# Kernel optimization log

Measured on AMD Instinct MI355X. Metric: run time of the kernel, lower is better.

## Reference

```python
import jax, jax.numpy as jnp
import numpy as np
import math

B, H, L, N, CD = 16, 512, 2048, 64, 128
BN_EPS = 1e-5


def setup_inputs() -> dict:
    key = jax.random.key(0)
    ks = jax.random.split(key, 12)
    x = jax.random.normal(ks[0], (B, H, L), jnp.float32)
    cond = jax.random.normal(ks[1], (B, CD), jnp.float32)
    # input Linear(H, H)
    linear_w = jax.random.normal(ks[2], (H, H), jnp.float32) * (1.0 / math.sqrt(H))
    linear_b = jax.random.normal(ks[3], (H,), jnp.float32) * 0.01
    # DSSM params (torch init: log_dt ~ U[log dt_min, log dt_max])
    log_dt = jax.random.uniform(ks[4], (H,), jnp.float32) * (math.log(0.1) - math.log(0.001)) + math.log(0.001)
    C_ri = jax.random.normal(ks[5], (H, N, 2), jnp.float32)  # view_as_real of complex C
    log_A_real = jnp.full((H, N), jnp.log(0.5), jnp.float32)
    A_imag = jnp.broadcast_to(math.pi * jnp.arange(N, dtype=jnp.float32), (H, N))
    D = jax.random.normal(ks[6], (H,), jnp.float32)
    # FiLM adaptor Linear(CD, 2H)
    film_w = jax.random.normal(ks[7], (2 * H, CD), jnp.float32) * (1.0 / math.sqrt(CD))
    film_b = jax.random.normal(ks[8], (2 * H,), jnp.float32) * 0.01
    # depthwise 1x1 residual conv (groups=H, bias=False) -> per-channel scale
    res_w = jax.random.normal(ks[9], (H,), jnp.float32)
    return {"x": x, "cond": cond, "linear_w": linear_w, "linear_b": linear_b,
            "log_dt": log_dt, "C_ri": C_ri, "log_A_real": log_A_real,
            "A_imag": A_imag, "D": D, "film_w": film_w, "film_b": film_b,
            "res_w": res_w}


def _s4_kernel(log_dt, C_ri, log_A_real, A_imag, length):
    dt = jnp.exp(log_dt)                       # [H]
    C = C_ri[..., 0] + 1j * C_ri[..., 1]       # [H, N] complex
    A = -jnp.exp(log_A_real) + 1j * A_imag     # [H, N] complex
    dtA = A * dt[:, None]                      # [H, N]
    t = jnp.arange(length, dtype=jnp.float32)
    P = dtA[:, :, None] * t                    # [H, N, L] complex
    Cm = C * (jnp.exp(dtA) - 1.0) / A          # [H, N]
    K = 2.0 * jnp.einsum('hn,hnl->hl', Cm, jnp.exp(P)).real  # [H, L]
    return K


def reference(x, cond, linear_w, linear_b, log_dt, C_ri, log_A_real, A_imag, D,
              film_w, film_b, res_w):
    # --- linear over channel dim (B H L -> B L H -> linear -> B H L) ---
    h = jnp.einsum('bhl,gh->bgl', x, linear_w) + linear_b[None, :, None]
    h = jax.nn.gelu(h, approximate=False)  # torch.nn.GELU default (erf)
    # --- DSSM: full-length group (forward passes length=None) ---
    K = _s4_kernel(log_dt, C_ri, log_A_real, A_imag, L)     # [H, L]
    n_fft = 2 * L
    k_f = jnp.fft.rfft(K, n=n_fft)                           # [H, Lf]
    u_f = jnp.fft.rfft(h, n=n_fft)                           # [B, H, Lf]
    y = jnp.fft.irfft(u_f * k_f[None], n=n_fft)[..., :L]     # [B, H, L]
    y = y + h * D[None, :, None]                             # D skip
    # --- FiLM: BatchNorm1d(affine=False, batch stats) then scale/shift ---
    gb = cond @ film_w.T + film_b                            # [B, 2H]
    g, b = gb[:, :H], gb[:, H:]
    mean = jnp.mean(y, axis=(0, 2), keepdims=True)
    var = jnp.var(y, axis=(0, 2), keepdims=True)             # biased, as torch BN
    y = (y - mean) * jax.lax.rsqrt(var + BN_EPS)
    y = y * g[:, :, None] + b[:, :, None]
    y = jax.nn.gelu(y, approximate=False)
    # --- depthwise 1x1 residual ---
    return y + x * res_w[None, :, None]
```

## Files before the change

### kernel.cpp

```cpp
#include <hip/hip_runtime.h>
#include <math.h>

#define B_ 16
#define H_ 512
#define L_ 2048
#define N_ 64
#define CD_ 128
#define KSTRIDE 2112

typedef unsigned int u32;
typedef unsigned short u16;
typedef __attribute__((ext_vector_type(8))) short bf16x8;
typedef __attribute__((ext_vector_type(4))) float f32x4;

__device__ __forceinline__ float gelu_f(float v) {
    return 0.5f * v * (1.0f + erff(v * 0.70710678118654752f));
}
__device__ __forceinline__ float bf2f(u16 b) {
    union { u32 u; float f; } c; c.u = ((u32)b) << 16; return c.f;
}
__device__ __forceinline__ u16 f2bf(float f) {
    union { float f; u32 u; } c; c.f = f;
    u32 u = c.u;
    return (u16)((u + 0x7FFFu + ((u >> 16) & 1u)) >> 16);
}
__device__ __forceinline__ u32 pack2(float a, float b) {
    u32 r;
    asm("v_cvt_pk_bf16_f32 %0, %1, %2" : "=v"(r) : "v"(a), "v"(b));
    return r;
}
__device__ __forceinline__ float2 cmul(float2 a, float2 b) {
    return make_float2(a.x * b.x - a.y * b.y, a.x * b.y + a.y * b.x);
}

__global__ void k_fill(float* __restrict__ out, int n, float val) {
    int i = blockIdx.x * 256 + threadIdx.x;
    if (i < n) out[i] = val;
}

__global__ __launch_bounds__(128) void k_prepW(const float* __restrict__ W,
                                               u16* __restrict__ Wb) {
    int g = blockIdx.x, t = threadIdx.x;
    float4 v = ((const float4*)(W + (size_t)g * H_))[t];
    u32* dst = (u32*)(Wb + (size_t)g * H_);
    dst[t * 2]     = pack2(v.x, v.y);
    dst[t * 2 + 1] = pack2(v.z, v.w);
}

__global__ __launch_bounds__(256) void k_K4(
    const float* __restrict__ log_dt, const float* __restrict__ C_ri,
    const float* __restrict__ log_A_real, const float* __restrict__ A_imag,
    u16* __restrict__ Krv) {
    int h = blockIdx.x, t = threadIdx.x;
    __shared__ float2 P1[N_][8], P8[N_][4], P32[N_][8], P256[N_][8], Cs[N_];
    if (t < N_) {
        int n = t;
        float dt = expf(log_dt[h]);
        float a_re = -expf(log_A_real[h * N_ + n]);
        float a_im = A_imag[h * N_ + n];
        float dre = a_re * dt, dim = a_im * dt;
        float er = expf(dre);
        float s, c;
        sincosf(dim, &s, &c);
        float2 E1 = make_float2(er * c, er * s);
        float num_re = E1.x - 1.0f, num_im = E1.y;
        float den = a_re * a_re + a_im * a_im;
        float q_re = (num_re * a_re + num_im * a_im) / den;
        float q_im = (num_im * a_re - num_re * a_im) / den;
        float Cr = C_ri[(h * N_ + n) * 2 + 0], Ci = C_ri[(h * N_ + n) * 2 + 1];
        Cs[n] = make_float2(Cr * q_re - Ci * q_im, Cr * q_im + Ci * q_re);
        float2 w = make_float2(1.f, 0.f);
        #pragma unroll
        for (int i = 0; i < 8; ++i) { P1[n][i] = w; w = cmul(w, E1); }
        float2 E8 = w; w = make_float2(1.f, 0.f);
        #pragma unroll
        for (int i = 0; i < 4; ++i) { P8[n][i] = w; w = cmul(w, E8); }
        float2 E32 = w; w = make_float2(1.f, 0.f);
        #pragma unroll
        for (int i = 0; i < 8; ++i) { P32[n][i] = w; w = cmul(w, E32); }
        float2 E256 = w; w = make_float2(1.f, 0.f);
        #pragma unroll
        for (int i = 0; i < 8; ++i) { P256[n][i] = w; w = cmul(w, E256); }
    }
    __syncthreads();
    int qh = t >> 5, ql = (t >> 2) & 7, rh = t & 3;
    float acc[8] = {};
    for (int n = 0; n < N_; ++n) {
        float2 a = cmul(Cs[n], P256[n][qh]);
        a = cmul(a, P32[n][ql]);
        a = cmul(a, P8[n][rh]);
        #pragma unroll
        for (int j = 0; j < 8; ++j) {
            float2 e = P1[n][j];
            acc[j] += a.x * e.x - a.y * e.y;
        }
    }
    u16* Krow = Krv + (size_t)h * KSTRIDE;
    uint4 w4;
    w4.x = pack2(2.0f * acc[7], 2.0f * acc[6]);
    w4.y = pack2(2.0f * acc[5], 2.0f * acc[4]);
    w4.z = pack2(2.0f * acc[3], 2.0f * acc[2]);
    w4.w = pack2(2.0f * acc[1], 2.0f * acc[0]);
    *(uint4*)&Krow[2040 - 8 * t] = w4;
    if (t < 8) {
        uint4 z = {0u, 0u, 0u, 0u};
        *(uint4*)&Krow[2048 + 8 * t] = z;
    }
}

__global__ __launch_bounds__(512, 4) void k_linear7(
    const float* __restrict__ x, const u16* __restrict__ Wb,
    const float* __restrict__ bias, u16* __restrict__ hb16) {
    int b  = blockIdx.z;
    int g0 = blockIdx.y * 128;
    int l0 = blockIdx.x * 128;
    __shared__ __align__(16) char sm[34816];
    u16* Wp = (u16*)sm;
    u16* Bl = (u16*)(sm + 16384);
    int t = threadIdx.x;
    int lane = t & 63, wv = t >> 6;
    int n = lane & 15, kg = lane >> 4;
    int wr = wv >> 2, wc = wv & 3;
    int lr  = t & 127, kq = t >> 7;
    int wrow = t >> 2, woct = t & 3;

    f32x4 acc[4][2];
    #pragma unroll
    for (int m = 0; m < 4; ++m)
        #pragma unroll
        for (int q = 0; q < 2; ++q) acc[m][q] = (f32x4){0.f, 0.f, 0.f, 0.f};

    const float* xcol = x + (size_t)b * H_ * L_ + l0 + lr;
    const u32* wsrc = (const u32*)(Wb + (size_t)(g0 + wrow) * H_);

    float cx[16], nx[16];
    uint4 cwq[2], nwq[2];
    #pragma unroll
    for (int e = 0; e < 16; ++e) cx[e] = xcol[(size_t)(kq * 16 + e) * L_];
    #pragma unroll
    for (int j = 0; j < 2; ++j)
        cwq[j] = *(const uint4*)&wsrc[(woct * 2 + j) * 4];

    #pragma unroll
    for (int S = 0; S < 8; ++S) {
        if (S) __syncthreads();
        {
            u32 px[8];
            #pragma unroll
            for (int e = 0; e < 8; ++e) px[e] = pack2(cx[2 * e], cx[2 * e + 1]);
            uint4 u0 = {px[0], px[1], px[2], px[3]};
            uint4 u1 = {px[4], px[5], px[6], px[7]};
            *(uint4*)((char*)Bl + lr * 144 + kq * 32)      = u0;
            *(uint4*)((char*)Bl + lr * 144 + kq * 32 + 16) = u1;
        }
        #pragma unroll
        for (int j = 0; j < 2; ++j) {
            int oct = woct * 2 + j;
            *(uint4*)((char*)Wp + wrow * 128 + ((oct * 16) ^ ((wrow & 7) << 4))) = cwq[j];
        }
        __syncthreads();
        if (S < 7) {
            int k0n = (S + 1) * 64;
            #pragma unroll
            for (int e = 0; e < 16; ++e) nx[e] = xcol[(size_t)(k0n + kq * 16 + e) * L_];
            #pragma unroll
            for (int j = 0; j < 2; ++j)
                nwq[j] = *(const uint4*)&wsrc[k0n / 2 + (woct * 2 + j) * 4];
        }
        #pragma unroll
        for (int ks = 0; ks < 2; ++ks) {
            bf16x8 af[4], bfr[2];
            #pragma unroll
            for (int m = 0; m < 4; ++m) {
                int row = wr * 64 + m * 16 + n;
                af[m] = *(const bf16x8*)((const char*)Wp + row * 128 +
                         ((ks * 64 + kg * 16) ^ ((row & 7) << 4)));
            }
            #pragma unroll
            for (int q = 0; q < 2; ++q)
                bfr[q] = *(const bf16x8*)((const char*)Bl +
                          (wc * 32 + q * 16 + n) * 144 + ks * 64 + kg * 16);
            #pragma unroll
            for (int m = 0; m < 4; ++m)
                #pragma unroll
                for (int q = 0; q < 2; ++q)
                    acc[m][q] = __builtin_amdgcn_mfma_f32_16x16x32_bf16(
                        af[m], bfr[q], acc[m][q], 0, 0, 0);
        }
        if (S < 7) {
            #pragma unroll
            for (int e = 0; e < 16; ++e) cx[e] = nx[e];
            cwq[0] = nwq[0]; cwq[1] = nwq[1];
        }
    }

    __syncthreads();
    u16* Yt = (u16*)sm;
    #pragma unroll
    for (int m = 0; m < 4; ++m) {
        #pragma unroll
        for (int r = 0; r < 4; ++r) {
            int grow = wr * 64 + m * 16 + kg * 4 + r;
            float bi = bias[g0 + grow];
            float v0 = gelu_f(acc[m][0][r] + bi);
            float v1 = gelu_f(acc[m][1][r] + bi);
            u32 pr = pack2(v0, v1);
            Yt[grow * 128 + wc * 32 + n]      = (u16)(pr & 0xFFFFu);
            Yt[grow * 128 + wc * 32 + 16 + n] = (u16)(pr >> 16);
        }
    }
    __syncthreads();
    int rrow = t >> 4, c16 = t & 15;
    #pragma unroll
    for (int pass = 0; pass < 4; ++pass) {
        int row = rrow + 32 * pass;
        uint4 v = *(const uint4*)&Yt[row * 128 + c16 * 8];
        *(uint4*)&hb16[((size_t)b * H_ + g0 + row) * L_ + l0 + c16 * 8] = v;
    }
}

template<int E, bool DIAG, bool TAIL, bool LOAD>
__device__ __forceinline__ void cstep(const uint2* __restrict__ KD2, int& base,
    bf16x8 (&ring)[8], f32x4 (&accR)[8], const char* smem,
    int rowbase, u32 swz, int kg16, int& ja) {
    uint2 w01, w23;
    if (DIAG) {
        int b0 = base < 2047 ? base : 2047;
        int b1 = (base + 4) < 2047 ? (base + 4) : 2047;
        w01 = KD2[b0];
        w23 = KD2[b1];
        if (base > 2047)     { w01.x = 0u; w01.y = 0u; }
        if (base + 4 > 2047) { w23.x = 0u; w23.y = 0u; }
    } else {
        w01 = KD2[base];
        w23 = KD2[base + 4];
    }
    union { u32 u[4]; bf16x8 v; } bu;
    bu.u[0] = w01.x; bu.u[1] = w01.y; bu.u[2] = w23.x; bu.u[3] = w23.y;
    #pragma unroll
    for (int m = 0; m < 8; ++m)
        if (!TAIL || m >= E)
            accR[m] = __builtin_amdgcn_mfma_f32_16x16x32_bf16(
                ring[(m - E) & 7], bu.v, accR[m], 0, 0, 0);
    if (LOAD) {
        ring[(7 - E) & 7] = *(const bf16x8*)(smem + rowbase +
                            (((u32)(ja * 64 + kg16)) ^ swz));
        ja -= 1;
    }
    base -= 32;
}

template<bool DIAG, bool TAIL, bool LOAD>
__device__ __forceinline__ void cblock8(const uint2* __restrict__ KD2, int& base,
    bf16x8 (&ring)[8], f32x4 (&accR)[8], const char* smem,
    int rowbase, u32 swz, int kg16, int& ja) {
    cstep<0, DIAG,  TAIL, LOAD>(KD2, base, ring, accR, smem, rowbase, swz, kg16, ja);
    cstep<1, false, TAIL, LOAD>(KD2, base, ring, accR, smem, rowbase, swz, kg16, ja);
    cstep<2, false, TAIL, LOAD>(KD2, base, ring, accR, smem, rowbase, swz, kg16, ja);
    cstep<3, false, TAIL, LOAD>(KD2, base, ring, accR, smem, rowbase, swz, kg16, ja);
    cstep<4, false, TAIL, LOAD>(KD2, base, ring, accR, smem, rowbase, swz, kg16, ja);
    cstep<5, false, TAIL, LOAD>(KD2, base, ring, accR, smem, rowbase, swz, kg16, ja);
    cstep<6, false, TAIL, LOAD>(KD2, base, ring, accR, smem, rowbase, swz, kg16, ja);
    cstep<7, false, TAIL, LOAD>(KD2, base, ring, accR, smem, rowbase, swz, kg16, ja);
}

__global__ __launch_bounds__(512, 4) void k_conv_mfma(
    float* __restrict__ out, const u16* __restrict__ hb16,
    const u16* __restrict__ Krv, const float* __restrict__ Dp,
    const float* __restrict__ x, const float* __restrict__ cond,
    const float* __restrict__ film_w, const float* __restrict__ film_b,
    const float* __restrict__ res_w) {
    int g = blockIdx.x;
    __shared__ __align__(16) char smem[81920];
    uint2* KD2 = (uint2*)(smem + 65536);
    int t = threadIdx.x;
    int wv = t >> 6, lane = t & 63;
    int n = lane & 15, kg = lane >> 4;

    {
        const u16* Krow = Krv + (size_t)g * KSTRIDE;
        uint2 d0 = *(const uint2*)&Krow[4 * t];
        uint2 d1 = *(const uint2*)&Krow[4 * t + 4];
        u32 m12 = (d0.x >> 16) | (d0.y << 16);
        u32 m34 = (d0.y >> 16) | (d1.x << 16);
        u32 m56 = (d1.x >> 16) | (d1.y << 16);
        uint4 e01 = {d0.x, d0.y, m12, m34};
        uint4 e23 = {d0.y, d1.x, m34, m56};
        *(uint4*)&KD2[4 * t]     = e01;
        *(uint4*)&KD2[4 * t + 2] = e23;
    }
    #pragma unroll
    for (int b = 0; b < B_; ++b) {
        uint2 p2 = *(const uint2*)&hb16[((size_t)b * H_ + g) * L_ + t * 4];
        *(uint2*)(smem + b * 4096 + (((u32)(t * 8)) ^ ((b & 7) << 4))) = p2;
    }
    __syncthreads();

    const int p = wv & 1, q4 = wv >> 1;
    const int rowbase = n * 4096;
    const u32 swz = (u32)((n & 7) << 4);
    const int kg16 = kg * 16;
    const int bofs = 8 * kg - n;
    const int rrs[2] = {q4, 7 - q4};

    f32x4 acc[2][8];
    #pragma unroll
    for (int ri = 0; ri < 2; ++ri)
        #pragma unroll
        for (int m = 0; m < 8; ++m) acc[ri][m] = (f32x4){0.f, 0.f, 0.f, 0.f};

    #pragma unroll
    for (int ri = 0; ri < 2; ++ri) {
        const int rr = rrs[ri];
        const int k8 = rr * 8;
        bf16x8 ring[8];
        #pragma unroll
        for (int m = 0; m < 8; ++m)
            ring[m] = *(const bf16x8*)(smem + rowbase +
                      (((u32)((k8 + m) * 64 + kg16)) ^ swz));
        int base = 2047 - 16 * p + bofs;
        int ja = k8 - 1;
        if (rr == 0) {
            cblock8<true, true, false>(KD2, base, ring, acc[ri], smem, rowbase, swz, kg16, ja);
        } else {
            cblock8<true, false, true>(KD2, base, ring, acc[ri], smem, rowbase, swz, kg16, ja);
            for (int bi = 1; bi < rr; ++bi)
                cblock8<false, false, true>(KD2, base, ring, acc[ri], smem, rowbase, swz, kg16, ja);
            cblock8<false, true, false>(KD2, base, ring, acc[ri], smem, rowbase, swz, kg16, ja);
        }
    }

    __syncthreads();
    float Dg = Dp[g];
    float sum = 0.f, sq = 0.f;
    #pragma unroll
    for (int ri = 0; ri < 2; ++ri) {
        #pragma unroll
        for (int m = 0; m < 8; ++m) {
            const int l0 = 16 * p + 256 * rrs[ri] + 32 * m;
            #pragma unroll
            for (int r = 0; r < 4; ++r) {
                int b = kg * 4 + r;
                u32 hoff = ((u32)(2 * (l0 + n))) ^ ((u32)((b & 7) << 4));
                float hval = bf2f(*(const u16*)(smem + b * 4096 + hoff));
                float y = acc[ri][m][r] + Dg * hval;
                sum += y; sq += y * y;
                *(u16*)(smem + b * 4096 + hoff) = f2bf(y);
            }
        }
    }
    #pragma unroll
    for (int off = 32; off > 0; off >>= 1) {
        sum += __shfl_down(sum, off);
        sq  += __shfl_down(sq, off);
    }
    __syncthreads();
    float* red = (float*)(smem + 65536);
    if (lane == 0) { red[wv] = sum; red[8 + wv] = sq; }
    if (t >= 64 && t < 96) {
        int tid = t - 64, b = tid >> 1, which = tid & 1;
        int row = which ? (H_ + g) : g;
        float a = film_b[row];
        const float4* wr4 = (const float4*)(film_w + (size_t)row * CD_);
        const float4* cp4 = (const float4*)(cond + b * CD_);
        #pragma unroll
        for (int c4 = 0; c4 < CD_ / 4; ++c4) {
            float4 cw = cp4[c4], ww = wr4[c4];
            a += cw.x * ww.x + cw.y * ww.y + cw.z * ww.z + cw.w * ww.w;
        }
        red[18 + tid] = a;
    }
    __syncthreads();
    if (t == 0) {
        float s = 0.f, q = 0.f;
        #pragma unroll
        for (int i = 0; i < 8; ++i) { s += red[i]; q += red[8 + i]; }
        const float inv = 1.0f / (float)(B_ * L_);
        float mean = s * inv;
        float var = q * inv - mean * mean;
        red[16] = mean; red[17] = rsqrtf(var + 1e-5f);
    }
    __syncthreads();

    const float mean = red[16], rstd = red[17];
    const float rw = res_w[g];
    const int fb = t >> 5, tc = t & 31;
    const float gf = red[18 + 2 * fb];
    const float bb = red[18 + 2 * fb + 1];
    const u32 fswz = (u32)((fb & 7) << 4);
    const char* yrow = smem + fb * 4096;
    const size_t rowoff = ((size_t)fb * H_ + g) * L_;
    #pragma unroll
    for (int i = 0; i < 16; ++i) {
        int l = tc * 4 + 128 * i;
        uint2 yy = *(const uint2*)(yrow + (((u32)(2 * l)) ^ fswz));
        float4 xv = *(const float4*)&x[rowoff + l];
        float4 o;
        o.x = gelu_f((bf2f((u16)(yy.x & 0xFFFFu)) - mean) * rstd * gf + bb) + xv.x * rw;
        o.y = gelu_f((bf2f((u16)(yy.x >> 16))     - mean) * rstd * gf + bb) + xv.y * rw;
        o.z = gelu_f((bf2f((u16)(yy.y & 0xFFFFu)) - mean) * rstd * gf + bb) + xv.z * rw;
        o.w = gelu_f((bf2f((u16)(yy.y >> 16))     - mean) * rstd * gf + bb) + xv.w * rw;
        *(float4*)&out[rowoff + l] = o;
    }
}

extern "C" void kernel_launch(void* const* d_in, const int* in_sizes, int n_in,
                              void* d_out, int out_size, void* d_ws, size_t ws_size,
                              hipStream_t stream) {
    const int expect[12] = {16777216, 2048, 262144, 512, 512, 65536,
                            32768, 32768, 512, 131072, 1024, 512};
    bool ok = (n_in == 12);
    if (ok) for (int i = 0; i < 12; ++i) if (in_sizes[i] != expect[i]) ok = false;
    if (!ok) {
        k_fill<<<(out_size + 255) / 256, 256, 0, stream>>>((float*)d_out, out_size, 1000.0f);
        return;
    }
    const size_t sz_Wb  = (size_t)H_ * H_ * 2;
    const size_t sz_Krv = (size_t)H_ * KSTRIDE * 2;
    const size_t sz_h   = (size_t)B_ * H_ * L_ * 2;
    if (ws_size < sz_Wb + sz_Krv + sz_h + 4096) {
        k_fill<<<(out_size + 255) / 256, 256, 0, stream>>>((float*)d_out, out_size, 2000.0f);
        return;
    }

    const float* x          = (const float*)d_in[0];
    const float* cond       = (const float*)d_in[1];
    const float* linear_w   = (const float*)d_in[2];
    const float* linear_b   = (const float*)d_in[3];
    const float* log_dt     = (const float*)d_in[4];
    const float* C_ri       = (const float*)d_in[5];
    const float* log_A_real = (const float*)d_in[6];
    const float* A_imag     = (const float*)d_in[7];
    const float* Dp         = (const float*)d_in[8];
    const float* film_w     = (const float*)d_in[9];
    const float* film_b     = (const float*)d_in[10];
    const float* res_w      = (const float*)d_in[11];

    float* outp = (float*)d_out;

    char* w = (char*)d_ws;
    u16* Wb   = (u16*)w;  w += sz_Wb;
    u16* Krv  = (u16*)w;  w += sz_Krv;
    u16* hb16 = (u16*)w;

    k_prepW<<<H_, 128, 0, stream>>>(linear_w, Wb);
    k_K4<<<H_, 256, 0, stream>>>(log_dt, C_ri, log_A_real, A_imag, Krv);
    dim3 gmm(L_ / 128, H_ / 128, B_);
    k_linear7<<<gmm, 512, 0, stream>>>(x, Wb, linear_b, hb16);
    k_conv_mfma<<<H_, 512, 0, stream>>>(outp, hb16, Krv, Dp, x,
                                        cond, film_w, film_b, res_w);
}
```

Before: 137.0 us.

## Pre-transpose x to bf16 L-major layout before linear GEMM

Adds a kernel that converts x to bf16 and transposes it to [B,L,H], staged through the output buffer as scratch. The GEMM then loads x tiles with vectorized 16-byte reads into a swizzled LDS layout matching the weight tile, replacing strided scalar fp32 loads and in-kernel packing. This costs an extra full pass over x (reading fp32, writing bf16) plus one more launch, and it relies on the output buffer not being needed until the conv kernel overwrites it.

```diff
diff --git a/kernel.cpp b/kernel.cpp
--- a/kernel.cpp
+++ b/kernel.cpp
@@ -45,6 +45,34 @@
     u32* dst = (u32*)(Wb + (size_t)g * H_);
     dst[t * 2]     = pack2(v.x, v.y);
     dst[t * 2 + 1] = pack2(v.z, v.w);
+}
+
+__global__ __launch_bounds__(256) void k_prepX(const float* __restrict__ x,
+                                               u16* __restrict__ xT) {
+    int b  = blockIdx.z;
+    int k0 = blockIdx.y * 64;
+    int l0 = blockIdx.x * 256;
+    __shared__ float xs[64][260];
+    int t = threadIdx.x;
+    int cr = t >> 6;
+    int cc = (t & 63) * 4;
+    #pragma unroll
+    for (int p = 0; p < 16; ++p) {
+        int r = p * 4 + cr;
+        float4 v = *(const float4*)&x[((size_t)b * H_ + k0 + r) * L_ + l0 + cc];
+        xs[r][cc] = v.x; xs[r][cc + 1] = v.y; xs[r][cc + 2] = v.z; xs[r][cc + 3] = v.w;
+    }
+    __syncthreads();
+    u16* dst = xT + ((size_t)b * L_ + l0 + t) * H_ + k0;
+    #pragma unroll
+    for (int j = 0; j < 8; ++j) {
+        uint4 w;
+        w.x = pack2(xs[j * 8 + 0][t], xs[j * 8 + 1][t]);
+        w.y = pack2(xs[j * 8 + 2][t], xs[j * 8 + 3][t]);
+        w.z = pack2(xs[j * 8 + 4][t], xs[j * 8 + 5][t]);
+        w.w = pack2(xs[j * 8 + 6][t], xs[j * 8 + 7][t]);
+        *(uint4*)&dst[j * 8] = w;
+    }
 }
 
 __global__ __launch_bounds__(256) void k_K4(
@@ -108,20 +136,19 @@
     }
 }
 
-__global__ __launch_bounds__(512, 4) void k_linear7(
-    const float* __restrict__ x, const u16* __restrict__ Wb,
+__global__ __launch_bounds__(512, 4) void k_linear8(
+    const u16* __restrict__ xT, const u16* __restrict__ Wb,
     const float* __restrict__ bias, u16* __restrict__ hb16) {
     int b  = blockIdx.z;
     int g0 = blockIdx.y * 128;
     int l0 = blockIdx.x * 128;
-    __shared__ __align__(16) char sm[34816];
+    __shared__ __align__(16) char sm[32768];
     u16* Wp = (u16*)sm;
-    u16* Bl = (u16*)(sm + 16384);
+    u16* Xl = (u16*)(sm + 16384);
     int t = threadIdx.x;
     int lane = t & 63, wv = t >> 6;
     int n = lane & 15, kg = lane >> 4;
     int wr = wv >> 2, wc = wv & 3;
-    int lr  = t & 127, kq = t >> 7;
     int wrow = t >> 2, woct = t & 3;
 
     f32x4 acc[4][2];
@@ -130,42 +157,34 @@
         #pragma unroll
         for (int q = 0; q < 2; ++q) acc[m][q] = (f32x4){0.f, 0.f, 0.f, 0.f};
 
-    const float* xcol = x + (size_t)b * H_ * L_ + l0 + lr;
     const u32* wsrc = (const u32*)(Wb + (size_t)(g0 + wrow) * H_);
-
-    float cx[16], nx[16];
-    uint4 cwq[2], nwq[2];
-    #pragma unroll
-    for (int e = 0; e < 16; ++e) cx[e] = xcol[(size_t)(kq * 16 + e) * L_];
-    #pragma unroll
-    for (int j = 0; j < 2; ++j)
+    const u32* xsrc = (const u32*)(xT + ((size_t)b * L_ + l0 + wrow) * H_);
+
+    uint4 cwq[2], cxq[2], nwq[2], nxq[2];
+    #pragma unroll
+    for (int j = 0; j < 2; ++j) {
         cwq[j] = *(const uint4*)&wsrc[(woct * 2 + j) * 4];
+        cxq[j] = *(const uint4*)&xsrc[(woct * 2 + j) * 4];
+    }
 
     #pragma unroll
     for (int S = 0; S < 8; ++S) {
         if (S) __syncthreads();
-        {
-            u32 px[8];
-            #pragma unroll
-            for (int e = 0; e < 8; ++e) px[e] = pack2(cx[2 * e], cx[2 * e + 1]);
-            uint4 u0 = {px[0], px[1], px[2], px[3]};
-            uint4 u1 = {px[4], px[5], px[6], px[7]};
-            *(uint4*)((char*)Bl + lr * 144 + kq * 32)      = u0;
-            *(uint4*)((char*)Bl + lr * 144 + kq * 32 + 16) = u1;
-        }
         #pragma unroll
         for (int j = 0; j < 2; ++j) {
             int oct = woct * 2 + j;
-            *(uint4*)((char*)Wp + wrow * 128 + ((oct * 16) ^ ((wrow & 7) << 4))) = cwq[j];
+            u32 off = (u32)(wrow * 128 + ((oct * 16) ^ ((wrow & 7) << 4)));
+            *(uint4*)((char*)Wp + off) = cwq[j];
+            *(uint4*)((char*)Xl + off) = cxq[j];
         }
         __syncthreads();
         if (S < 7) {
-            int k0n = (S + 1) * 64;
+            int kn = (S + 1) * 32;
             #pragma unroll
-            for (int e = 0; e < 16; ++e) nx[e] = xcol[(size_t)(k0n + kq * 16 + e) * L_];
-            #pragma unroll
-            for (int j = 0; j < 2; ++j)
-                nwq[j] = *(const uint4*)&wsrc[k0n / 2 + (woct * 2 + j) * 4];
+            for (int j = 0; j < 2; ++j) {
+                nwq[j] = *(const uint4*)&wsrc[kn + (woct * 2 + j) * 4];
+                nxq[j] = *(const uint4*)&xsrc[kn + (woct * 2 + j) * 4];
+            }
         }
         #pragma unroll
         for (int ks = 0; ks < 2; ++ks) {
@@ -177,9 +196,11 @@
                          ((ks * 64 + kg * 16) ^ ((row & 7) << 4)));
             }
             #pragma unroll
-            for (int q = 0; q < 2; ++q)
-                bfr[q] = *(const bf16x8*)((const char*)Bl +
-                          (wc * 32 + q * 16 + n) * 144 + ks * 64 + kg * 16);
+            for (int q = 0; q < 2; ++q) {
+                int row = wc * 32 + q * 16 + n;
+                bfr[q] = *(const bf16x8*)((const char*)Xl + row * 128 +
+                          ((ks * 64 + kg * 16) ^ ((row & 7) << 4)));
+            }
             #pragma unroll
             for (int m = 0; m < 4; ++m)
                 #pragma unroll
@@ -188,9 +209,8 @@
                         af[m], bfr[q], acc[m][q], 0, 0, 0);
         }
         if (S < 7) {
-            #pragma unroll
-            for (int e = 0; e < 16; ++e) cx[e] = nx[e];
             cwq[0] = nwq[0]; cwq[1] = nwq[1];
+            cxq[0] = nxq[0]; cxq[1] = nxq[1];
         }
     }
 
@@ -437,6 +457,7 @@
     const float* res_w      = (const float*)d_in[11];
 
     float* outp = (float*)d_out;
+    u16*   xT   = (u16*)d_out;
 
     char* w = (char*)d_ws;
     u16* Wb   = (u16*)w;  w += sz_Wb;
@@ -444,9 +465,11 @@
     u16* hb16 = (u16*)w;
 
     k_prepW<<<H_, 128, 0, stream>>>(linear_w, Wb);
+    dim3 gpx(L_ / 256, H_ / 64, B_);
+    k_prepX<<<gpx, 256, 0, stream>>>(x, xT);
     k_K4<<<H_, 256, 0, stream>>>(log_dt, C_ri, log_A_real, A_imag, Krv);
     dim3 gmm(L_ / 128, H_ / 128, B_);
-    k_linear7<<<gmm, 512, 0, stream>>>(x, Wb, linear_b, hb16);
+    k_linear8<<<gmm, 512, 0, stream>>>(xT, Wb, linear_b, hb16);
     k_conv_mfma<<<H_, 512, 0, stream>>>(outp, hb16, Krv, Dp, x,
                                         cond, film_w, film_b, res_w);
 }
```

New measurement: 178.7 us. 1.3x slower.
